# Kernel optimization log

Measured on AMD Instinct MI355X. Metric: run time of the kernel, lower is better.

The kernel has to match this reference:

```python
import jax, jax.numpy as jnp
import numpy as np

NUM_HEADS = 16
D_MODEL = 1024
D_K = D_MODEL // NUM_HEADS


def setup_inputs() -> dict:
    key = jax.random.key(0)
    ks = jax.random.split(key, 11)
    B, S, D = 4, 2048, D_MODEL
    s = 1.0 / np.sqrt(D)
    return {
        "query": jax.random.normal(ks[0], (B, S, D), jnp.float32),
        "key": jax.random.normal(ks[1], (B, S, D), jnp.float32),
        "value": jax.random.normal(ks[2], (B, S, D), jnp.float32),
        "Wq": jax.random.normal(ks[3], (D, D), jnp.float32) * s,
        "bq": jnp.zeros((D,), jnp.float32),
        "Wk": jax.random.normal(ks[4], (D, D), jnp.float32) * s,
        "bk": jnp.zeros((D,), jnp.float32),
        "Wv": jax.random.normal(ks[5], (D, D), jnp.float32) * s,
        "bv": jnp.zeros((D,), jnp.float32),
        "Wo": jax.random.normal(ks[6], (D, D), jnp.float32) * s,
        "bo": jnp.zeros((D,), jnp.float32),
    }


def reference(query, key, value, Wq, bq, Wk, bk, Wv, bv, Wo, bo):
    B, S, D = query.shape
    H, dk = NUM_HEADS, D_K
    # linear projections (torch Linear: x @ W.T + b)
    q = query @ Wq.T + bq
    k = key @ Wk.T + bk
    v = value @ Wv.T + bv
    # [B, S, D] -> [B, H, S, dk]
    q = q.reshape(B, S, H, dk).transpose(0, 2, 1, 3)
    k = k.reshape(B, S, H, dk).transpose(0, 2, 1, 3)
    v = v.reshape(B, S, H, dk).transpose(0, 2, 1, 3)
    # scaled dot-product attention (explicit scores, no mask, dropout unused in fwd)
    scores = jnp.einsum("bhqd,bhkd->bhqk", q, k) / jnp.sqrt(jnp.float32(dk))
    attn = jax.nn.softmax(scores, axis=-1)
    out = jnp.einsum("bhqk,bhkd->bhqd", attn, v)
    out = out.transpose(0, 2, 1, 3).reshape(B, S, D)
    return out @ Wo.T + bo
```

## Files before the change

### kernel.cpp

```cpp
#include <hip/hip_runtime.h>
#include <cstdint>
#include <cstddef>

typedef __bf16 bf16_t;
typedef __bf16 bf16x8 __attribute__((ext_vector_type(8)));
typedef __bf16 bf16x4 __attribute__((ext_vector_type(4)));
typedef float f32x4 __attribute__((ext_vector_type(4)));

static constexpr int SEQ = 2048;
static constexpr int DMODEL = 1024;
static constexpr int HEADS = 16;
static constexpr int DK = 64;
static constexpr int MROWS = 4 * SEQ;
static constexpr size_t NEC = (size_t)MROWS * DMODEL;
static constexpr size_t WEC = (size_t)DMODEL * DMODEL;

__global__ __launch_bounds__(256) void cast_w(const float* __restrict__ wq,
                                              const float* __restrict__ wk,
                                              const float* __restrict__ wv,
                                              const float* __restrict__ wo,
                                              bf16_t* __restrict__ out) {
  size_t i = (size_t)blockIdx.x * 256 + threadIdx.x;
  size_t e = i * 8;
  const float* src;
  size_t off;
  if (e < WEC) { src = wq; off = e; }
  else if (e < 2 * WEC) { src = wk; off = e - WEC; }
  else if (e < 3 * WEC) { src = wv; off = e - 2 * WEC; }
  else { src = wo; off = e - 3 * WEC; }
  const float4* p = reinterpret_cast<const float4*>(src + off);
  float4 a = p[0], b = p[1];
  bf16x8 o;
  o[0] = (bf16_t)a.x; o[1] = (bf16_t)a.y; o[2] = (bf16_t)a.z; o[3] = (bf16_t)a.w;
  o[4] = (bf16_t)b.x; o[5] = (bf16_t)b.y; o[6] = (bf16_t)b.z; o[7] = (bf16_t)b.w;
  *(reinterpret_cast<bf16x8*>(out + e)) = o;
}

__device__ __forceinline__ void async16(const void* g, void* l) {
  __builtin_amdgcn_global_load_lds((const __attribute__((address_space(1))) void*)g,
                                   (__attribute__((address_space(3))) void*)l,
                                   16, 0, 0);
}

__device__ __forceinline__ int lds_off(int m, int l4) {
  int lr = m >> 1;
  return lr * 64 + (((((m & 1) << 2) | l4) ^ (lr & 7)) << 3);
}

__global__ __launch_bounds__(512, 4) void gemm_qkv(const float* __restrict__ Aq,
                                                   const float* __restrict__ Ak,
                                                   const float* __restrict__ Av,
                                                   const bf16_t* __restrict__ Wbase,
                                                   const float* __restrict__ bq,
                                                   const float* __restrict__ bk,
                                                   const float* __restrict__ bv,
                                                   float scaleQ,
                                                   bf16_t* __restrict__ QKbase,
                                                   bf16_t* __restrict__ Vt) {
  __shared__ __align__(16) bf16_t smem[24576];
  float* sAf = reinterpret_cast<float*>(smem);
  bf16_t* sBb = smem + 16384;
  const int tid = threadIdx.x;
  const int lane = tid & 63;
  const int w = tid >> 6;
  const int wm = w >> 2, wn = w & 3;
  const int l16 = lane & 15, l4 = lane >> 4;
  const int sub8 = lane >> 3, c8 = lane & 7;

  int bid = blockIdx.x;
  int swz = (bid & 7) * 96 + (bid >> 3);
  const int seg = swz >> 8;
  const int inner = swz & 255;
  const float* Afp = seg == 0 ? Aq : (seg == 1 ? Ak : Av);
  const bf16_t* Bw = Wbase + (size_t)seg * WEC;
  const float* bias = seg == 0 ? bq : (seg == 1 ? bk : bv);
  const float scale = seg == 0 ? scaleQ : 1.0f;
  const int bm = inner >> 2, bn = inner & 3;
  const int m0 = bm << 7, n0 = bn << 8;

  const int sg = c8 ^ sub8;
  const int mS = 2 * (w * 8 + sub8) + (sg >> 2);
  const int gS = (sg & 3) * 8;
  const int rA = w * 8 + sub8;
  const int gA = (c8 ^ sub8) * 4;

  f32x4 acc[4][4] = {};

  auto stageA = [&](int bb, int k0) {
#pragma unroll
    for (int c = 0; c < 2; ++c)
      async16(Afp + (size_t)(m0 + c * 64 + rA) * DMODEL + k0 + gA,
              sAf + bb * 4096 + c * 2048 + w * 256);
  };
  auto stageB = [&](int k0) {
    async16(Bw + (size_t)(n0 + mS) * DMODEL + k0 + gS, sBb + w * 512);
    async16(Bw + (size_t)(n0 + 128 + mS) * DMODEL + k0 + gS, sBb + 4096 + w * 512);
  };

  stageA(0, 0);
  stageB(0);
  __syncthreads();
  const int NKT = DMODEL / 32;
  for (int t = 0; t < NKT; ++t) {
    bf16x8 bf[4];
#pragma unroll
    for (int j = 0; j < 4; ++j)
      bf[j] = *reinterpret_cast<const bf16x8*>(&sBb[lds_off(wn * 64 + j * 16 + l16, l4)]);
    __syncthreads();
    if (t + 1 < NKT) {
      stageA((t + 1) & 1, (t + 1) * 32);
      stageB((t + 1) * 32);
    }
    const float* bA = sAf + (t & 1) * 4096;
    bf16x8 af[4];
#pragma unroll
    for (int f = 0; f < 4; ++f) {
      int R = wm * 64 + f * 16 + l16;
      int s0 = (2 * l4) ^ (R & 7);
      const float* rb = bA + R * 32;
      f32x4 a0 = *reinterpret_cast<const f32x4*>(rb + s0 * 4);
      f32x4 a1 = *reinterpret_cast<const f32x4*>(rb + (s0 ^ 1) * 4);
#pragma unroll
      for (int e = 0; e < 4; ++e) { af[f][e] = (bf16_t)a0[e]; af[f][4 + e] = (bf16_t)a1[e]; }
    }
    __builtin_amdgcn_s_setprio(1);
#pragma unroll
    for (int i = 0; i < 4; ++i)
#pragma unroll
      for (int j = 0; j < 4; ++j)
        acc[i][j] = __builtin_amdgcn_mfma_f32_16x16x32_bf16(af[i], bf[j], acc[i][j], 0, 0, 0);
    __builtin_amdgcn_s_setprio(0);
    __syncthreads();
  }

  float bj[4];
#pragma unroll
  for (int j = 0; j < 4; ++j) bj[j] = bias[n0 + wn * 64 + j * 16 + l16];

  const int hglob = bn * 4 + wn;
  bf16_t* patch = smem + w * 3072;

  if (seg < 2) {
    bf16_t* outQK = QKbase + (size_t)seg * NEC;
#pragma unroll
    for (int h2 = 0; h2 < 2; ++h2) {
#pragma unroll
      for (int ii = 0; ii < 2; ++ii) {
        int i = h2 * 2 + ii;
#pragma unroll
        for (int j = 0; j < 4; ++j) {
#pragma unroll
          for (int r = 0; r < 4; ++r) {
            float v = (acc[i][j][r] + bj[j]) * scale;
            patch[(ii * 16 + l4 * 4 + r) * 72 + j * 16 + l16] = (bf16_t)v;
          }
        }
      }
#pragma unroll
      for (int kk = 0; kk < 4; ++kk) {
        int row = kk * 8 + sub8;
        int doff = c8 * 8;
        bf16x8 ch = *reinterpret_cast<const bf16x8*>(&patch[row * 72 + doff]);
        int m = m0 + wm * 64 + h2 * 32 + row;
        int b = m >> 11, s = m & 2047;
        *reinterpret_cast<bf16x8*>(
            &outQK[(((size_t)(b * HEADS + hglob) * SEQ + s) << 6) + doff]) = ch;
      }
    }
  } else {
#pragma unroll
    for (int h2 = 0; h2 < 2; ++h2) {
#pragma unroll
      for (int ii = 0; ii < 2; ++ii) {
        int i = h2 * 2 + ii;
#pragma unroll
        for (int j = 0; j < 4; ++j) {
          bf16x4 pk;
#pragma unroll
          for (int r = 0; r < 4; ++r) pk[r] = (bf16_t)(acc[i][j][r] + bj[j]);
          *reinterpret_cast<bf16x4*>(
              &patch[(j * 16 + l16) * 48 + ii * 16 + l4 * 4]) = pk;
        }
      }
#pragma unroll
      for (int kk = 0; kk < 4; ++kk) {
        int d = kk * 16 + (lane >> 2);
        int soff = (lane & 3) * 8;
        bf16x8 ch = *reinterpret_cast<const bf16x8*>(&patch[d * 48 + soff]);
        int m = m0 + wm * 64 + h2 * 32;
        int b = m >> 11, s = (m & 2047) + soff;
        *reinterpret_cast<bf16x8*>(
            &Vt[((size_t)(b * HEADS + hglob) * DK + d) * SEQ + s]) = ch;
      }
    }
  }
}

__global__ __launch_bounds__(256, 4) void gemm_out(const bf16_t* __restrict__ A,
                                                   const bf16_t* __restrict__ Bw,
                                                   const float* __restrict__ bias,
                                                   float* __restrict__ Cout) {
  __shared__ __align__(16) bf16_t sA[2][128 * 32];
  __shared__ __align__(16) bf16_t sB[2][128 * 32];
  const int tid = threadIdx.x;
  const int lane = tid & 63;
  const int wv = tid >> 6;
  const int l16 = lane & 15, l4 = lane >> 4;

  int bid = blockIdx.x;
  int swz = (bid & 7) * 64 + (bid >> 3);
  const int bm = swz >> 3, bn = swz & 7;
  const int m0 = bm << 7, n0 = bn << 7;
  const int wr = (wv >> 1) * 64, wc = (wv & 1) * 64;

  const int sg = (lane & 7) ^ ((lane >> 3) & 7);
  const int mS = 2 * (wv * 8 + (lane >> 3)) + (sg >> 2);
  const int gS = (sg & 3) * 8;

  f32x4 acc[4][4] = {};

  auto stage = [&](int bb, int k0) {
#pragma unroll
    for (int c = 0; c < 2; ++c) {
      async16(A + (size_t)(m0 + c * 64 + mS) * DMODEL + k0 + gS, &sA[bb][c * 2048 + wv * 512]);
      async16(Bw + (size_t)(n0 + c * 64 + mS) * DMODEL + k0 + gS, &sB[bb][c * 2048 + wv * 512]);
    }
  };

  stage(0, 0);
  __syncthreads();
  const int NKT = DMODEL / 32;
  for (int t = 0; t < NKT; ++t) {
    if (t + 1 < NKT) stage((t + 1) & 1, (t + 1) * 32);
    const bf16_t* bA = sA[t & 1];
    const bf16_t* bB = sB[t & 1];
    bf16x8 afrag[4], bfrag[4];
#pragma unroll
    for (int f = 0; f < 4; ++f) {
      afrag[f] = *reinterpret_cast<const bf16x8*>(&bA[lds_off(wr + f * 16 + l16, l4)]);
      bfrag[f] = *reinterpret_cast<const bf16x8*>(&bB[lds_off(wc + f * 16 + l16, l4)]);
    }
    __builtin_amdgcn_s_setprio(1);
#pragma unroll
    for (int i = 0; i < 4; ++i)
#pragma unroll
      for (int j = 0; j < 4; ++j)
        acc[i][j] = __builtin_amdgcn_mfma_f32_16x16x32_bf16(afrag[i], bfrag[j], acc[i][j], 0, 0, 0);
    __builtin_amdgcn_s_setprio(0);
    __syncthreads();
  }

  float bj[4];
#pragma unroll
  for (int j = 0; j < 4; ++j) bj[j] = bias[n0 + wc + j * 16 + l16];

#pragma unroll
  for (int i = 0; i < 4; ++i) {
#pragma unroll
    for (int j = 0; j < 4; ++j) {
#pragma unroll
      for (int r = 0; r < 4; ++r) {
        int m = m0 + wr + i * 16 + l4 * 4 + r;
        int n = n0 + wc + j * 16 + l16;
        Cout[(size_t)m * DMODEL + n] = acc[i][j][r] + bj[j];
      }
    }
  }
}

__device__ __forceinline__ int kvsrc_row(int r) {
  return (r & 32) | (((r >> 3) & 1) << 4) | (((r >> 2) & 1) << 3) |
         (((r >> 4) & 1) << 2) | (r & 3);
}

__global__ __launch_bounds__(512, 2) void attn_kernel(const bf16_t* __restrict__ Q,
                                                      const bf16_t* __restrict__ Kp,
                                                      const bf16_t* __restrict__ Vt,
                                                      bf16_t* __restrict__ AO) {
  __shared__ __align__(16) bf16_t sK[2][64 * 64];
  __shared__ __align__(16) bf16_t sV[2][64 * 64];
  const int tid = threadIdx.x;
  const int lane = tid & 63;
  const int wv = tid >> 6;
  const int l16 = lane & 15, l4 = lane >> 4;
  const int sub8 = lane >> 3, c8 = lane & 7;

  const int nq = SEQ / 256;
  int bid = blockIdx.x;
  int swz = (bid & 7) * 64 + (bid >> 3);
  const int bh = swz / nq, qt = swz % nq;
  const int b = bh >> 4, h = bh & 15;
  const bf16_t* Qh = Q + (size_t)bh * SEQ * DK;
  const bf16_t* Kh = Kp + (size_t)bh * SEQ * DK;
  const bf16_t* Vh = Vt + (size_t)bh * DK * SEQ;
  const int q0 = qt * 256 + wv * 32;

  bf16x8 aq[2][2];
#pragma unroll
  for (int s = 0; s < 2; ++s)
#pragma unroll
    for (int hf = 0; hf < 2; ++hf)
      aq[s][hf] = *reinterpret_cast<const bf16x8*>(
          &Qh[(size_t)(q0 + s * 16 + l16) * DK + hf * 32 + l4 * 8]);

  bf16x8 ones;
#pragma unroll
  for (int i = 0; i < 8; ++i) ones[i] = (bf16_t)1.0f;

  f32x4 o[2][4] = {};
  f32x4 lacc[2] = {};

  auto stage = [&](int buf, int kv0) {
    int r = wv * 8 + sub8;
    int kvr = kvsrc_row(r);
    int cs = (c8 ^ sub8) << 3;
    async16(Kh + (size_t)(kv0 + kvr) * DK + cs, &sK[buf][wv * 512]);
    async16(Vh + (size_t)r * SEQ + kv0 + cs, &sV[buf][wv * 512]);
  };

  auto compute = [&](int buf) {
    const bf16_t* bK = sK[buf];
    const bf16_t* bV = sV[buf];
    f32x4 sc[2][4] = {};
    __builtin_amdgcn_s_setprio(1);
#pragma unroll
    for (int t = 0; t < 4; ++t) {
      bf16x8 kf0 = *reinterpret_cast<const bf16x8*>(
          &bK[(t * 16 + l16) * 64 + ((l4 ^ (l16 & 7)) << 3)]);
      bf16x8 kf1 = *reinterpret_cast<const bf16x8*>(
          &bK[(t * 16 + l16) * 64 + (((4 + l4) ^ (l16 & 7)) << 3)]);
#pragma unroll
      for (int s = 0; s < 2; ++s) {
        sc[s][t] = __builtin_amdgcn_mfma_f32_16x16x32_bf16(kf0, aq[s][0], sc[s][t], 0, 0, 0);
        sc[s][t] = __builtin_amdgcn_mfma_f32_16x16x32_bf16(kf1, aq[s][1], sc[s][t], 0, 0, 0);
      }
    }
    __builtin_amdgcn_s_setprio(0);
    bf16x8 pa[2][2];
#pragma unroll
    for (int s = 0; s < 2; ++s) {
#pragma unroll
      for (int t = 0; t < 4; ++t) {
#pragma unroll
        for (int j = 0; j < 4; ++j) {
          pa[s][t >> 1][(t & 1) * 4 + j] = (bf16_t)__builtin_amdgcn_exp2f(sc[s][t][j]);
        }
      }
    }
    __builtin_amdgcn_s_setprio(1);
#pragma unroll
    for (int nb = 0; nb < 4; ++nb) {
      bf16x8 vf0 = *reinterpret_cast<const bf16x8*>(
          &bV[(nb * 16 + l16) * 64 + ((l4 ^ (l16 & 7)) << 3)]);
      bf16x8 vf1 = *reinterpret_cast<const bf16x8*>(
          &bV[(nb * 16 + l16) * 64 + (((4 + l4) ^ (l16 & 7)) << 3)]);
#pragma unroll
      for (int s = 0; s < 2; ++s) {
        o[s][nb] = __builtin_amdgcn_mfma_f32_16x16x32_bf16(pa[s][0], vf0, o[s][nb], 0, 0, 0);
        o[s][nb] = __builtin_amdgcn_mfma_f32_16x16x32_bf16(pa[s][1], vf1, o[s][nb], 0, 0, 0);
      }
    }
#pragma unroll
    for (int s = 0; s < 2; ++s) {
      lacc[s] = __builtin_amdgcn_mfma_f32_16x16x32_bf16(pa[s][0], ones, lacc[s], 0, 0, 0);
      lacc[s] = __builtin_amdgcn_mfma_f32_16x16x32_bf16(pa[s][1], ones, lacc[s], 0, 0, 0);
    }
    __builtin_amdgcn_s_setprio(0);
  };

  stage(0, 0);
  __syncthreads();
  const int NT = SEQ / 64;
  for (int it = 0; it < NT; ++it) {
    if (it + 1 < NT) stage((it + 1) & 1, (it + 1) * 64);
    compute(it & 1);
    __syncthreads();
  }

#pragma unroll
  for (int s = 0; s < 2; ++s) {
#pragma unroll
    for (int j = 0; j < 4; ++j) {
      float inv = 1.0f / lacc[s][j];
      int qrow = q0 + s * 16 + l4 * 4 + j;
#pragma unroll
      for (int nb = 0; nb < 4; ++nb)
        AO[((size_t)(b * SEQ + qrow)) * DMODEL + h * DK + nb * 16 + l16] =
            (bf16_t)(o[s][nb][j] * inv);
    }
  }
}

extern "C" void kernel_launch(void* const* d_in, const int* in_sizes, int n_in,
                              void* d_out, int out_size, void* d_ws, size_t ws_size,
                              hipStream_t stream) {
  const float* query = (const float*)d_in[0];
  const float* key_i = (const float*)d_in[1];
  const float* value = (const float*)d_in[2];
  const float* Wq = (const float*)d_in[3];
  const float* bq = (const float*)d_in[4];
  const float* Wk = (const float*)d_in[5];
  const float* bk = (const float*)d_in[6];
  const float* Wv = (const float*)d_in[7];
  const float* bv = (const float*)d_in[8];
  const float* Wo = (const float*)d_in[9];
  const float* bo = (const float*)d_in[10];
  float* out = (float*)d_out;

  bf16_t* wqb = (bf16_t*)d_ws;
  bf16_t* wob = wqb + 3 * WEC;
  bf16_t* Qp = wob + WEC;
  bf16_t* Kp = Qp + NEC;
  bf16_t* Vt = Kp + NEC;
  bf16_t* AO = Vt + NEC;

  cast_w<<<dim3((unsigned)(4 * WEC / 8 / 256)), dim3(256), 0, stream>>>(
      Wq, Wk, Wv, Wo, wqb);

  const float cexp = 0.18033688f;
  gemm_qkv<<<dim3(768), dim3(512), 0, stream>>>(query, key_i, value, wqb,
                                                bq, bk, bv, cexp, Qp, Vt);

  attn_kernel<<<dim3(4 * HEADS * (SEQ / 256)), 512, 0, stream>>>(Qp, Kp, Vt, AO);

  gemm_out<<<dim3(512), dim3(256), 0, stream>>>(AO, wob, bo, out);
}
```

Measured before the change: 166.8 us.

## Halve attention query tile to 16 rows per wave and raise occupancy

The attention kernel now gives each wave 16 query rows instead of 32, so a block covers 128 queries and the grid doubles to 1024 blocks. Launch bounds ask for up to 8 blocks per CU, and the KV loop is unrolled by two with fixed buffer indices. The aim is more resident waves to hide latency and less register pressure per wave. In exchange, each K/V tile loaded into LDS is reused by half as many query rows, so K/V traffic and staging overhead per FLOP roughly double.

After: 181.6 us. 1.09x slower.

```diff
diff --git a/kernel.cpp b/kernel.cpp
--- a/kernel.cpp
+++ b/kernel.cpp
@@ -273,7 +273,7 @@
          (((r >> 4) & 1) << 2) | (r & 3);
 }
 
-__global__ __launch_bounds__(512, 2) void attn_kernel(const bf16_t* __restrict__ Q,
+__global__ __launch_bounds__(512, 8) void attn_kernel(const bf16_t* __restrict__ Q,
                                                       const bf16_t* __restrict__ Kp,
                                                       const bf16_t* __restrict__ Vt,
                                                       bf16_t* __restrict__ AO) {
@@ -285,30 +285,28 @@
   const int l16 = lane & 15, l4 = lane >> 4;
   const int sub8 = lane >> 3, c8 = lane & 7;
 
-  const int nq = SEQ / 256;
+  const int nq = SEQ / 128;
   int bid = blockIdx.x;
-  int swz = (bid & 7) * 64 + (bid >> 3);
+  int swz = (bid & 7) * 128 + (bid >> 3);
   const int bh = swz / nq, qt = swz % nq;
   const int b = bh >> 4, h = bh & 15;
   const bf16_t* Qh = Q + (size_t)bh * SEQ * DK;
   const bf16_t* Kh = Kp + (size_t)bh * SEQ * DK;
   const bf16_t* Vh = Vt + (size_t)bh * DK * SEQ;
-  const int q0 = qt * 256 + wv * 32;
-
-  bf16x8 aq[2][2];
-#pragma unroll
-  for (int s = 0; s < 2; ++s)
-#pragma unroll
-    for (int hf = 0; hf < 2; ++hf)
-      aq[s][hf] = *reinterpret_cast<const bf16x8*>(
-          &Qh[(size_t)(q0 + s * 16 + l16) * DK + hf * 32 + l4 * 8]);
+  const int q0 = qt * 128 + wv * 16;
+
+  bf16x8 aq[2];
+#pragma unroll
+  for (int hf = 0; hf < 2; ++hf)
+    aq[hf] = *reinterpret_cast<const bf16x8*>(
+        &Qh[(size_t)(q0 + l16) * DK + hf * 32 + l4 * 8]);
 
   bf16x8 ones;
 #pragma unroll
   for (int i = 0; i < 8; ++i) ones[i] = (bf16_t)1.0f;
 
-  f32x4 o[2][4] = {};
-  f32x4 lacc[2] = {};
+  f32x4 o[4] = {};
+  f32x4 lacc = {};
 
   auto stage = [&](int buf, int kv0) {
     int r = wv * 8 + sub8;
@@ -318,10 +316,8 @@
     async16(Vh + (size_t)r * SEQ + kv0 + cs, &sV[buf][wv * 512]);
   };
 
-  auto compute = [&](int buf) {
-    const bf16_t* bK = sK[buf];
-    const bf16_t* bV = sV[buf];
-    f32x4 sc[2][4] = {};
+  auto compute = [&](const bf16_t* bK, const bf16_t* bV) {
+    f32x4 sc[4] = {};
     __builtin_amdgcn_s_setprio(1);
 #pragma unroll
     for (int t = 0; t < 4; ++t) {
@@ -329,22 +325,16 @@
           &bK[(t * 16 + l16) * 64 + ((l4 ^ (l16 & 7)) << 3)]);
       bf16x8 kf1 = *reinterpret_cast<const bf16x8*>(
           &bK[(t * 16 + l16) * 64 + (((4 + l4) ^ (l16 & 7)) << 3)]);
-#pragma unroll
-      for (int s = 0; s < 2; ++s) {
-        sc[s][t] = __builtin_amdgcn_mfma_f32_16x16x32_bf16(kf0, aq[s][0], sc[s][t], 0, 0, 0);
-        sc[s][t] = __builtin_amdgcn_mfma_f32_16x16x32_bf16(kf1, aq[s][1], sc[s][t], 0, 0, 0);
-      }
+      sc[t] = __builtin_amdgcn_mfma_f32_16x16x32_bf16(kf0, aq[0], sc[t], 0, 0, 0);
+      sc[t] = __builtin_amdgcn_mfma_f32_16x16x32_bf16(kf1, aq[1], sc[t], 0, 0, 0);
     }
     __builtin_amdgcn_s_setprio(0);
-    bf16x8 pa[2][2];
-#pragma unroll
-    for (int s = 0; s < 2; ++s) {
-#pragma unroll
-      for (int t = 0; t < 4; ++t) {
-#pragma unroll
-        for (int j = 0; j < 4; ++j) {
-          pa[s][t >> 1][(t & 1) * 4 + j] = (bf16_t)__builtin_amdgcn_exp2f(sc[s][t][j]);
-        }
+    bf16x8 pa[2];
+#pragma unroll
+    for (int t = 0; t < 4; ++t) {
+#pragma unroll
+      for (int j = 0; j < 4; ++j) {
+        pa[t >> 1][(t & 1) * 4 + j] = (bf16_t)__builtin_amdgcn_exp2f(sc[t][j]);
       }
     }
     __builtin_amdgcn_s_setprio(1);
@@ -354,40 +344,34 @@
           &bV[(nb * 16 + l16) * 64 + ((l4 ^ (l16 & 7)) << 3)]);
       bf16x8 vf1 = *reinterpret_cast<const bf16x8*>(
           &bV[(nb * 16 + l16) * 64 + (((4 + l4) ^ (l16 & 7)) << 3)]);
-#pragma unroll
-      for (int s = 0; s < 2; ++s) {
-        o[s][nb] = __builtin_amdgcn_mfma_f32_16x16x32_bf16(pa[s][0], vf0, o[s][nb], 0, 0, 0);
-        o[s][nb] = __builtin_amdgcn_mfma_f32_16x16x32_bf16(pa[s][1], vf1, o[s][nb], 0, 0, 0);
-      }
-    }
-#pragma unroll
-    for (int s = 0; s < 2; ++s) {
-      lacc[s] = __builtin_amdgcn_mfma_f32_16x16x32_bf16(pa[s][0], ones, lacc[s], 0, 0, 0);
-      lacc[s] = __builtin_amdgcn_mfma_f32_16x16x32_bf16(pa[s][1], ones, lacc[s], 0, 0, 0);
-    }
+      o[nb] = __builtin_amdgcn_mfma_f32_16x16x32_bf16(pa[0], vf0, o[nb], 0, 0, 0);
+      o[nb] = __builtin_amdgcn_mfma_f32_16x16x32_bf16(pa[1], vf1, o[nb], 0, 0, 0);
+    }
+    lacc = __builtin_amdgcn_mfma_f32_16x16x32_bf16(pa[0], ones, lacc, 0, 0, 0);
+    lacc = __builtin_amdgcn_mfma_f32_16x16x32_bf16(pa[1], ones, lacc, 0, 0, 0);
     __builtin_amdgcn_s_setprio(0);
   };
 
   stage(0, 0);
   __syncthreads();
   const int NT = SEQ / 64;
-  for (int it = 0; it < NT; ++it) {
-    if (it + 1 < NT) stage((it + 1) & 1, (it + 1) * 64);
-    compute(it & 1);
+  for (int it = 0; it < NT; it += 2) {
+    stage(1, (it + 1) * 64);
+    compute(sK[0], sV[0]);
     __syncthreads();
-  }
-
-#pragma unroll
-  for (int s = 0; s < 2; ++s) {
-#pragma unroll
-    for (int j = 0; j < 4; ++j) {
-      float inv = 1.0f / lacc[s][j];
-      int qrow = q0 + s * 16 + l4 * 4 + j;
-#pragma unroll
-      for (int nb = 0; nb < 4; ++nb)
-        AO[((size_t)(b * SEQ + qrow)) * DMODEL + h * DK + nb * 16 + l16] =
-            (bf16_t)(o[s][nb][j] * inv);
-    }
+    if (it + 2 < NT) stage(0, (it + 2) * 64);
+    compute(sK[1], sV[1]);
+    __syncthreads();
+  }
+
+#pragma unroll
+  for (int j = 0; j < 4; ++j) {
+    float inv = 1.0f / lacc[j];
+    int qrow = q0 + l4 * 4 + j;
+#pragma unroll
+    for (int nb = 0; nb < 4; ++nb)
+      AO[((size_t)(b * SEQ + qrow)) * DMODEL + h * DK + nb * 16 + l16] =
+          (bf16_t)(o[nb][j] * inv);
   }
 }
 
@@ -421,7 +405,7 @@
   gemm_qkv<<<dim3(768), dim3(512), 0, stream>>>(query, key_i, value, wqb,
                                                 bq, bk, bv, cexp, Qp, Vt);
 
-  attn_kernel<<<dim3(4 * HEADS * (SEQ / 256)), 512, 0, stream>>>(Qp, Kp, Vt, AO);
+  attn_kernel<<<dim3(4 * HEADS * (SEQ / 128)), 512, 0, stream>>>(Qp, Kp, Vt, AO);
 
   gemm_out<<<dim3(512), dim3(256), 0, stream>>>(AO, wob, bo, out);
 }
```
